# Kernel tuning notes

Measured on AMD Instinct MI355X. Metric: run time of the kernel, lower is better.

The kernel has to match this reference:

```python
import jax, jax.numpy as jnp
import numpy as np

B, C, H, W = 4, 128, 64, 64
NUM_HEADS = 4
HEAD_DIM = C // NUM_HEADS


def setup_inputs() -> dict:
    key = jax.random.key(0)
    ks = jax.random.split(key, 9)
    s = 0.02
    return {
        "x": jax.random.normal(ks[0], (B, C, H, W), dtype=jnp.float32),
        "wq": jax.random.normal(ks[1], (C, C), dtype=jnp.float32) * s,
        "bq": jax.random.normal(ks[2], (C,), dtype=jnp.float32) * s,
        "wk": jax.random.normal(ks[3], (C, C), dtype=jnp.float32) * s,
        "bk": jax.random.normal(ks[4], (C,), dtype=jnp.float32) * s,
        "wv": jax.random.normal(ks[5], (C, C), dtype=jnp.float32) * s,
        "bv": jax.random.normal(ks[6], (C,), dtype=jnp.float32) * s,
        "wo": jax.random.normal(ks[7], (C, C), dtype=jnp.float32) * s,
        "bo": jax.random.normal(ks[8], (C,), dtype=jnp.float32) * s,
    }


def _proj(w, b, xf):
    # 1x1 conv == channel-mixing linear: xf is (B, C, N)
    return jnp.einsum("oc,bcn->bon", w, xf) + b[None, :, None]


def reference(x, wq, bq, wk, bk, wv, bv, wo, bo):
    b, c, h, w = x.shape
    n = h * w
    nh, hd = NUM_HEADS, HEAD_DIM
    xf = x.reshape(b, c, n)
    q = _proj(wq, bq, xf).reshape(b, nh, hd, n)
    k = _proj(wk, bk, xf).reshape(b, nh, hd, n)
    v = _proj(wv, bv, xf).reshape(b, nh, hd, n)
    # scores: (b, heads, n, n)
    scores = jnp.einsum("bhdn,bhdm->bhnm", q, k) / jnp.sqrt(jnp.float32(hd)).astype(x.dtype)
    prob = jax.nn.softmax(scores, axis=-1)
    # attn_out: (b, heads, head_dim, n)
    attn = jnp.einsum("bhnm,bhdm->bhdn", prob, v).reshape(b, c, n)
    out = _proj(wo, bo, attn).reshape(b, c, h, w)
    return x + out
```

## Files before the change

### kernel.cpp

```cpp
#include <hip/hip_runtime.h>
#include <hip/hip_bf16.h>

#define BB 4
#define CC 128
#define NN 4096
#define NHEAD 4
#define HDIM 32
#define KSPLIT 2

typedef short bf16x8_t __attribute__((ext_vector_type(8)));
typedef float f32x4_t __attribute__((ext_vector_type(4)));
typedef int i32x4_t __attribute__((ext_vector_type(4)));

#define MFMA16(a, b, c) __builtin_amdgcn_mfma_f32_16x16x32_bf16(a, b, c, 0, 0, 0)
#define EXP2(x) __builtin_amdgcn_exp2f(x)

#define QSCALE (0.17677669529663687f * 1.4426950408889634f)

static __device__ inline unsigned short f2bf(float f) {
  unsigned u = __builtin_bit_cast(unsigned, f);
  u += 0x7fffu + ((u >> 16) & 1u);
  return (unsigned short)(u >> 16);
}
static __device__ inline unsigned pk2(float lo, float hi) {
  return (unsigned)f2bf(lo) | ((unsigned)f2bf(hi) << 16);
}
static __device__ inline unsigned pack_trunc(float lo, float hi) {
  return __builtin_amdgcn_perm(__builtin_bit_cast(unsigned, hi),
                               __builtin_bit_cast(unsigned, lo), 0x07060302u);
}

static __device__ inline void gload_lds16(const unsigned short* gsrc, void* ldst) {
  __builtin_amdgcn_global_load_lds(
      (const __attribute__((address_space(1))) unsigned int*)gsrc,
      (__attribute__((address_space(3))) unsigned int*)ldst, 16, 0, 0);
}

__global__ __launch_bounds__(256) void wconv_kernel(
    const float* __restrict__ wq, const float* __restrict__ wk,
    const float* __restrict__ wv, const float* __restrict__ wo,
    unsigned short* __restrict__ wb) {
  int f = (blockIdx.x * 256 + threadIdx.x) * 8;
  int m = f >> 14, off = f & 16383;
  const float* src = (m == 0) ? wq : (m == 1) ? wk : (m == 2) ? wv : wo;
  float sc = (m == 0) ? QSCALE : 1.0f;
  float4 a = *(const float4*)(src + off);
  float4 b = *(const float4*)(src + off + 4);
  ushort4 u0, u1;
  u0.x = f2bf(a.x * sc); u0.y = f2bf(a.y * sc); u0.z = f2bf(a.z * sc); u0.w = f2bf(a.w * sc);
  u1.x = f2bf(b.x * sc); u1.y = f2bf(b.y * sc); u1.z = f2bf(b.z * sc); u1.w = f2bf(b.w * sc);
  *(ushort4*)(wb + f) = u0;
  *(ushort4*)(wb + f + 4) = u1;
}

__global__ __launch_bounds__(256) void qkv_mfma_kernel(
    const float* __restrict__ x,
    const unsigned short* __restrict__ wqb, const unsigned short* __restrict__ wkb,
    const unsigned short* __restrict__ wvb,
    const float* __restrict__ bq, const float* __restrict__ bk,
    const float* __restrict__ bv,
    unsigned short* __restrict__ qt, unsigned short* __restrict__ kt,
    unsigned short* __restrict__ vg) {
  __shared__ __attribute__((aligned(16))) unsigned short xsb[64][136];
  __shared__ unsigned short vt[128][66];
  const int b = blockIdx.y, nt = blockIdx.x, proj = blockIdx.z;
  const int tid = threadIdx.x;

#pragma unroll
  for (int i = 0; i < 8; i++) {
    int f = tid + 256 * i;
    int c = f >> 4, n4 = (f & 15) * 4;
    float4 v4 = *(const float4*)(x + ((size_t)b * CC + c) * NN + nt * 64 + n4);
    xsb[n4 + 0][c] = f2bf(v4.x);
    xsb[n4 + 1][c] = f2bf(v4.y);
    xsb[n4 + 2][c] = f2bf(v4.z);
    xsb[n4 + 3][c] = f2bf(v4.w);
  }
  __syncthreads();

  const int lane = tid & 63, w = tid >> 6;
  const int l16 = lane & 15, g = lane >> 4;
  const int nl = w * 16;
  const int ngl = nt * 64 + nl;

  bf16x8_t xf[4];
#pragma unroll
  for (int ks = 0; ks < 4; ks++)
    xf[ks] = *(const bf16x8_t*)&xsb[nl + l16][ks * 32 + g * 8];

  const unsigned short* wm = (proj == 0) ? wqb : (proj == 1) ? wkb : wvb;
  const float* bias = (proj == 0) ? bq : (proj == 1) ? bk : bv;
  const float bsc = (proj == 0) ? QSCALE : 1.0f;
  unsigned short* qkdst = proj ? kt : qt;

#pragma unroll
  for (int ot = 0; ot < 8; ot++) {
    f32x4_t acc;
#pragma unroll
    for (int r = 0; r < 4; r++) acc[r] = bias[ot * 16 + g * 4 + r] * bsc;
#pragma unroll
    for (int ks = 0; ks < 4; ks++) {
      bf16x8_t wf = *(const bf16x8_t*)(wm + (size_t)(ot * 16 + l16) * CC + ks * 32 + g * 8);
      acc = MFMA16(wf, xf[ks], acc);
    }
    if (proj < 2) {
      unsigned p0 = pk2(acc[0], acc[1]);
      unsigned p1 = pk2(acc[2], acc[3]);
      unsigned q0 = (unsigned)__shfl_xor((int)p0, 16);
      unsigned q1 = (unsigned)__shfl_xor((int)p1, 16);
      if ((g & 1) == 0) {
        int hh = ot >> 1, dblk = (ot & 1) * 2 + (g >> 1);
        unsigned short* dst =
            qkdst + (((size_t)(b * NHEAD + hh) * 4 + dblk) * NN + ngl + l16) * 8;
        uint4 val = make_uint4(p0, p1, q0, q1);
        *(uint4*)dst = val;
      }
    } else {
#pragma unroll
      for (int r = 0; r < 4; r++) vt[ot * 16 + g * 4 + r][nl + l16] = f2bf(acc[r]);
    }
  }

  if (proj == 2) {
    __syncthreads();
#pragma unroll
    for (int c = 0; c < 4; c++) {
      int cid = c * 256 + tid;
      int hh = cid >> 8, inner = cid & 255;
      int g2 = inner & 3, l16v = (inner >> 2) & 15, fh = inner >> 6;
      int fv = fh >> 1, half = fh & 1;
      int o = hh * 32 + half * 16 + l16v;
      int n0 = fv * 32 + g2 * 4;
      unsigned d0 = *(const unsigned*)&vt[o][n0];
      unsigned d1 = *(const unsigned*)&vt[o][n0 + 2];
      unsigned d2 = *(const unsigned*)&vt[o][n0 + 16];
      unsigned d3 = *(const unsigned*)&vt[o][n0 + 18];
      uint4 val = make_uint4(d0, d1, d2, d3);
      *(uint4*)(vg + (((size_t)(b * NHEAD + hh) * 64 + nt) * 256 + inner) * 8) = val;
    }
  }
}

__global__ __launch_bounds__(256, 4) void attn_mfma5_kernel(
    const unsigned short* __restrict__ qt, const unsigned short* __restrict__ kt,
    const unsigned short* __restrict__ vg,
    float* __restrict__ opart, float* __restrict__ lpart) {
  __shared__ __attribute__((aligned(16))) unsigned short smem[2][4096];

  const int chunk = blockIdx.x & (KSPLIT - 1), nt = blockIdx.x / KSPLIT;
  const int h = blockIdx.y, b = blockIdx.z;
  const int bh = b * NHEAD + h;
  const int tid = threadIdx.x, lane = tid & 63, wid = tid >> 6;
  const int l16 = lane & 15, g = lane >> 4;
  const int nbase = nt * 128 + wid * 32;

  const unsigned short* qb = qt + (size_t)bh * NN * HDIM;
  const unsigned short* kb = kt + (size_t)bh * NN * HDIM;
  const unsigned short* vgb = vg + (size_t)bh * 64 * 2048;

  const bf16x8_t qf0 = *(const bf16x8_t*)(qb + ((size_t)g * NN + nbase + l16) * 8);
  const bf16x8_t qf1 = *(const bf16x8_t*)(qb + ((size_t)g * NN + nbase + 16 + l16) * 8);

  f32x4_t o00 = {0, 0, 0, 0}, o01 = {0, 0, 0, 0};
  f32x4_t o10 = {0, 0, 0, 0}, o11 = {0, 0, 0, 0};
  f32x4_t la = {0, 0, 0, 0}, lb = {0, 0, 0, 0};
  const f32x4_t zf = {0, 0, 0, 0};
  const i32x4_t onesi = {0x3F803F80, 0x3F803F80, 0x3F803F80, 0x3F803F80};
  const bf16x8_t ones = __builtin_bit_cast(bf16x8_t, onesi);

  const int NITER = 64 / KSPLIT;
  const int mt0 = chunk * NITER;

  const unsigned short* ksrc = kb + ((size_t)g * NN + mt0 * 64 + wid * 16 + l16) * 8;
  const unsigned short* vsrc = vgb + (size_t)mt0 * 2048 + (size_t)((wid * 16 + l16) * 4 + g) * 8;

  auto stage = [&](int p, int i) {
    gload_lds16(ksrc + (size_t)i * 512, &smem[p][wid * 512]);
    gload_lds16(vsrc + (size_t)i * 2048, &smem[p][2048 + wid * 512]);
  };

  auto body = [&](int p) {
    const unsigned short* sk = &smem[p][0];
    bf16x8_t k0 = *(const bf16x8_t*)(sk + 0 * 512 + lane * 8);
    bf16x8_t k1 = *(const bf16x8_t*)(sk + 1 * 512 + lane * 8);
    bf16x8_t k2 = *(const bf16x8_t*)(sk + 2 * 512 + lane * 8);
    bf16x8_t k3 = *(const bf16x8_t*)(sk + 3 * 512 + lane * 8);
    bf16x8_t vf0 = *(const bf16x8_t*)(sk + 2048 + 0 * 512 + lane * 8);
    bf16x8_t vf2 = *(const bf16x8_t*)(sk + 2048 + 1 * 512 + lane * 8);
    bf16x8_t vf1 = *(const bf16x8_t*)(sk + 2048 + 2 * 512 + lane * 8);
    bf16x8_t vf3 = *(const bf16x8_t*)(sk + 2048 + 3 * 512 + lane * 8);

    f32x4_t sA0 = MFMA16(k0, qf0, zf), sA1 = MFMA16(k1, qf0, zf);
    f32x4_t sA2 = MFMA16(k2, qf0, zf), sA3 = MFMA16(k3, qf0, zf);
    f32x4_t sB0 = MFMA16(k0, qf1, zf), sB1 = MFMA16(k1, qf1, zf);
    f32x4_t sB2 = MFMA16(k2, qf1, zf), sB3 = MFMA16(k3, qf1, zf);

#pragma unroll
    for (int r = 0; r < 4; r++) {
      sA0[r] = EXP2(sA0[r]); sA1[r] = EXP2(sA1[r]);
      sA2[r] = EXP2(sA2[r]); sA3[r] = EXP2(sA3[r]);
      sB0[r] = EXP2(sB0[r]); sB1[r] = EXP2(sB1[r]);
      sB2[r] = EXP2(sB2[r]); sB3[r] = EXP2(sB3[r]);
    }

    i32x4_t pA0i = {(int)pack_trunc(sA0[0], sA0[1]), (int)pack_trunc(sA0[2], sA0[3]),
                    (int)pack_trunc(sA1[0], sA1[1]), (int)pack_trunc(sA1[2], sA1[3])};
    i32x4_t pA1i = {(int)pack_trunc(sA2[0], sA2[1]), (int)pack_trunc(sA2[2], sA2[3]),
                    (int)pack_trunc(sA3[0], sA3[1]), (int)pack_trunc(sA3[2], sA3[3])};
    i32x4_t pB0i = {(int)pack_trunc(sB0[0], sB0[1]), (int)pack_trunc(sB0[2], sB0[3]),
                    (int)pack_trunc(sB1[0], sB1[1]), (int)pack_trunc(sB1[2], sB1[3])};
    i32x4_t pB1i = {(int)pack_trunc(sB2[0], sB2[1]), (int)pack_trunc(sB2[2], sB2[3]),
                    (int)pack_trunc(sB3[0], sB3[1]), (int)pack_trunc(sB3[2], sB3[3])};
    bf16x8_t pA0 = __builtin_bit_cast(bf16x8_t, pA0i);
    bf16x8_t pA1 = __builtin_bit_cast(bf16x8_t, pA1i);
    bf16x8_t pB0 = __builtin_bit_cast(bf16x8_t, pB0i);
    bf16x8_t pB1 = __builtin_bit_cast(bf16x8_t, pB1i);

    o00 = MFMA16(vf0, pA0, o00); o00 = MFMA16(vf1, pA1, o00);
    o01 = MFMA16(vf2, pA0, o01); o01 = MFMA16(vf3, pA1, o01);
    o10 = MFMA16(vf0, pB0, o10); o10 = MFMA16(vf1, pB1, o10);
    o11 = MFMA16(vf2, pB0, o11); o11 = MFMA16(vf3, pB1, o11);

    la = MFMA16(ones, pA0, la); la = MFMA16(ones, pA1, la);
    lb = MFMA16(ones, pB0, lb); lb = MFMA16(ones, pB1, lb);
  };

  stage(0, 0);
  __syncthreads();
  for (int mi = 0; mi < NITER; mi += 2) {
    stage(1, mi + 1);
    body(0);
    __syncthreads();
    if (mi + 2 < NITER) stage(0, mi + 2);
    body(1);
    __syncthreads();
  }

  float* obase = opart + ((size_t)(chunk * BB * NHEAD + bh)) * HDIM * NN;
#pragma unroll
  for (int r = 0; r < 4; r++) {
    obase[(size_t)(g * 4 + r) * NN + nbase + l16] = o00[r];
    obase[(size_t)(16 + g * 4 + r) * NN + nbase + l16] = o01[r];
    obase[(size_t)(g * 4 + r) * NN + nbase + 16 + l16] = o10[r];
    obase[(size_t)(16 + g * 4 + r) * NN + nbase + 16 + l16] = o11[r];
  }
  if (g == 0) {
    float* lb_ = lpart + (size_t)(chunk * BB * NHEAD + bh) * NN;
    lb_[nbase + l16] = la[0];
    lb_[nbase + 16 + l16] = lb[0];
  }
}

__global__ __launch_bounds__(256) void combine_kernel(
    const float* __restrict__ opart, const float* __restrict__ lpart,
    unsigned short* __restrict__ attnT) {
  const int n = blockIdx.x * 256 + threadIdx.x;
  const int bh = blockIdx.y, dg = blockIdx.z;
  const int b = bh >> 2, h = bh & 3;

  float l = 0.f;
#pragma unroll
  for (int c = 0; c < KSPLIT; c++) l += lpart[(size_t)(c * BB * NHEAD + bh) * NN + n];
  float inv = 1.f / l;

  unsigned dw[4];
#pragma unroll
  for (int p = 0; p < 4; p++) {
    float s0 = 0.f, s1 = 0.f;
#pragma unroll
    for (int c = 0; c < KSPLIT; c++) {
      const float* ob = opart + ((size_t)(c * BB * NHEAD + bh) * HDIM + dg * 8) * NN;
      s0 += ob[(size_t)(2 * p) * NN + n];
      s1 += ob[(size_t)(2 * p + 1) * NN + n];
    }
    dw[p] = (unsigned)f2bf(s0 * inv) | ((unsigned)f2bf(s1 * inv) << 16);
  }
  unsigned short* dst = attnT + ((size_t)b * NN + n) * CC + h * HDIM + dg * 8;
  *(uint4*)dst = *(uint4*)&dw[0];
}

__global__ __launch_bounds__(256) void out_mfma_kernel(
    const unsigned short* __restrict__ attnT, const unsigned short* __restrict__ wob,
    const float* __restrict__ bo, const float* __restrict__ x,
    float* __restrict__ out) {
  const int b = blockIdx.y, nt = blockIdx.x, quarter = blockIdx.z;
  const int tid = threadIdx.x, lane = tid & 63, w = tid >> 6;
  const int l16 = lane & 15, g = lane >> 4;
  const int n0 = nt * 64 + w * 16;

  bf16x8_t bf[4];
#pragma unroll
  for (int ks = 0; ks < 4; ks++)
    bf[ks] = *(const bf16x8_t*)(attnT + ((size_t)b * NN + n0 + l16) * CC + ks * 32 + g * 8);

#pragma unroll
  for (int mi = 0; mi < 2; mi++) {
    int mt = quarter * 2 + mi;
    f32x4_t acc;
#pragma unroll
    for (int r = 0; r < 4; r++) acc[r] = bo[mt * 16 + g * 4 + r];
#pragma unroll
    for (int ks = 0; ks < 4; ks++) {
      bf16x8_t af = *(const bf16x8_t*)(wob + (size_t)(mt * 16 + l16) * CC + ks * 32 + g * 8);
      acc = MFMA16(af, bf[ks], acc);
    }
#pragma unroll
    for (int r = 0; r < 4; r++) {
      int o = mt * 16 + g * 4 + r;
      size_t addr = ((size_t)b * CC + o) * NN + n0 + l16;
      out[addr] = acc[r] + x[addr];
    }
  }
}

extern "C" void kernel_launch(void* const* d_in, const int* in_sizes, int n_in,
                              void* d_out, int out_size, void* d_ws, size_t ws_size,
                              hipStream_t stream) {
  const float* x  = (const float*)d_in[0];
  const float* wq = (const float*)d_in[1];
  const float* bq = (const float*)d_in[2];
  const float* wk = (const float*)d_in[3];
  const float* bk = (const float*)d_in[4];
  const float* wv = (const float*)d_in[5];
  const float* bv = (const float*)d_in[6];
  const float* wo = (const float*)d_in[7];
  const float* bo = (const float*)d_in[8];
  float* out = (float*)d_out;

  char* w = (char*)d_ws;
  const size_t SZ = (size_t)BB * NHEAD * NN * HDIM * 2;
  unsigned short* qt    = (unsigned short*)w;
  unsigned short* kt    = (unsigned short*)(w + SZ);
  unsigned short* vg    = (unsigned short*)(w + 2 * SZ);
  unsigned short* wb    = (unsigned short*)(w + 3 * SZ);
  float* opart = (float*)(w + 3 * SZ + 131072);
  float* lpart = (float*)(w + 3 * SZ + 131072 +
                          (size_t)KSPLIT * BB * NHEAD * HDIM * NN * 4);
  unsigned short* attnT = qt;
  unsigned short* wqb = wb, *wkb = wb + 16384, *wvb = wb + 32768, *wob = wb + 49152;

  wconv_kernel<<<32, 256, 0, stream>>>(wq, wk, wv, wo, wb);
  qkv_mfma_kernel<<<dim3(NN / 64, BB, 3), 256, 0, stream>>>(
      x, wqb, wkb, wvb, bq, bk, bv, qt, kt, vg);
  attn_mfma5_kernel<<<dim3((NN / 128) * KSPLIT, NHEAD, BB), 256, 0, stream>>>(
      qt, kt, vg, opart, lpart);
  combine_kernel<<<dim3(NN / 256, BB * NHEAD, 4), 256, 0, stream>>>(opart, lpart, attnT);
  out_mfma_kernel<<<dim3(NN / 64, BB, 4), 256, 0, stream>>>(attnT, wob, bo, x, out);
}
```

Measured before the change: 147.0 us.

## Fuse split-K combine into output projection and precompute bf16 transposed x

Merges the combine kernel into the output-projection kernel: each 512-thread block sums the two split-K partials, normalizes by the summed softmax denominators, and stages the bf16 tile in shared memory before the MFMA. This removes a launch and the attnT round trip through global memory. Separately, x is converted to transposed bf16 once in a new xconv kernel, instead of being reconverted by each of the three projection blocks. That adds a launch and a bf16 copy of x, which reuses the opart buffer before the attention kernel overwrites it.

```diff
diff --git a/kernel.cpp b/kernel.cpp
--- a/kernel.cpp
+++ b/kernel.cpp
@@ -53,40 +53,52 @@
   *(ushort4*)(wb + f + 4) = u1;
 }
 
+__global__ __launch_bounds__(256) void xconv_kernel(
+    const float* __restrict__ x, unsigned short* __restrict__ xbT) {
+  __shared__ __attribute__((aligned(16))) unsigned short xs[64][136];
+  const int b = blockIdx.y, nt = blockIdx.x;
+  const int tid = threadIdx.x;
+#pragma unroll
+  for (int i = 0; i < 8; i++) {
+    int f = tid + 256 * i;
+    int c = f >> 4, n4 = (f & 15) * 4;
+    float4 v4 = *(const float4*)(x + ((size_t)b * CC + c) * NN + nt * 64 + n4);
+    xs[n4 + 0][c] = f2bf(v4.x);
+    xs[n4 + 1][c] = f2bf(v4.y);
+    xs[n4 + 2][c] = f2bf(v4.z);
+    xs[n4 + 3][c] = f2bf(v4.w);
+  }
+  __syncthreads();
+  unsigned short* dst = xbT + ((size_t)b * NN + nt * 64) * CC;
+#pragma unroll
+  for (int i = 0; i < 4; i++) {
+    int f = tid + 256 * i;
+    int n = f >> 4, c0 = (f & 15) * 8;
+    *(uint4*)(dst + f * 8) = *(const uint4*)&xs[n][c0];
+  }
+}
+
 __global__ __launch_bounds__(256) void qkv_mfma_kernel(
-    const float* __restrict__ x,
+    const unsigned short* __restrict__ xbT,
     const unsigned short* __restrict__ wqb, const unsigned short* __restrict__ wkb,
     const unsigned short* __restrict__ wvb,
     const float* __restrict__ bq, const float* __restrict__ bk,
     const float* __restrict__ bv,
     unsigned short* __restrict__ qt, unsigned short* __restrict__ kt,
     unsigned short* __restrict__ vg) {
-  __shared__ __attribute__((aligned(16))) unsigned short xsb[64][136];
   __shared__ unsigned short vt[128][66];
   const int b = blockIdx.y, nt = blockIdx.x, proj = blockIdx.z;
   const int tid = threadIdx.x;
-
-#pragma unroll
-  for (int i = 0; i < 8; i++) {
-    int f = tid + 256 * i;
-    int c = f >> 4, n4 = (f & 15) * 4;
-    float4 v4 = *(const float4*)(x + ((size_t)b * CC + c) * NN + nt * 64 + n4);
-    xsb[n4 + 0][c] = f2bf(v4.x);
-    xsb[n4 + 1][c] = f2bf(v4.y);
-    xsb[n4 + 2][c] = f2bf(v4.z);
-    xsb[n4 + 3][c] = f2bf(v4.w);
-  }
-  __syncthreads();
-
   const int lane = tid & 63, w = tid >> 6;
   const int l16 = lane & 15, g = lane >> 4;
   const int nl = w * 16;
   const int ngl = nt * 64 + nl;
 
+  const unsigned short* xrow = xbT + ((size_t)b * NN + ngl + l16) * CC + g * 8;
   bf16x8_t xf[4];
 #pragma unroll
   for (int ks = 0; ks < 4; ks++)
-    xf[ks] = *(const bf16x8_t*)&xsb[nl + l16][ks * 32 + g * 8];
+    xf[ks] = *(const bf16x8_t*)(xrow + ks * 32);
 
   const unsigned short* wm = (proj == 0) ? wqb : (proj == 1) ? wkb : wvb;
   const float* bias = (proj == 0) ? bq : (proj == 1) ? bk : bv;
@@ -251,58 +263,63 @@
   }
 }
 
-__global__ __launch_bounds__(256) void combine_kernel(
+__global__ __launch_bounds__(512) void out_mfma_kernel(
     const float* __restrict__ opart, const float* __restrict__ lpart,
-    unsigned short* __restrict__ attnT) {
-  const int n = blockIdx.x * 256 + threadIdx.x;
-  const int bh = blockIdx.y, dg = blockIdx.z;
-  const int b = bh >> 2, h = bh & 3;
-
-  float l = 0.f;
-#pragma unroll
-  for (int c = 0; c < KSPLIT; c++) l += lpart[(size_t)(c * BB * NHEAD + bh) * NN + n];
-  float inv = 1.f / l;
-
-  unsigned dw[4];
-#pragma unroll
-  for (int p = 0; p < 4; p++) {
-    float s0 = 0.f, s1 = 0.f;
-#pragma unroll
-    for (int c = 0; c < KSPLIT; c++) {
-      const float* ob = opart + ((size_t)(c * BB * NHEAD + bh) * HDIM + dg * 8) * NN;
-      s0 += ob[(size_t)(2 * p) * NN + n];
-      s1 += ob[(size_t)(2 * p + 1) * NN + n];
-    }
-    dw[p] = (unsigned)f2bf(s0 * inv) | ((unsigned)f2bf(s1 * inv) << 16);
-  }
-  unsigned short* dst = attnT + ((size_t)b * NN + n) * CC + h * HDIM + dg * 8;
-  *(uint4*)dst = *(uint4*)&dw[0];
-}
-
-__global__ __launch_bounds__(256) void out_mfma_kernel(
-    const unsigned short* __restrict__ attnT, const unsigned short* __restrict__ wob,
-    const float* __restrict__ bo, const float* __restrict__ x,
-    float* __restrict__ out) {
-  const int b = blockIdx.y, nt = blockIdx.x, quarter = blockIdx.z;
-  const int tid = threadIdx.x, lane = tid & 63, w = tid >> 6;
+    const unsigned short* __restrict__ wob, const float* __restrict__ bo,
+    const float* __restrict__ x, float* __restrict__ out) {
+  __shared__ __attribute__((aligned(16))) unsigned short xsb[64][136];
+  __shared__ float linv[NHEAD][64];
+  const int b = blockIdx.y, nt = blockIdx.x;
+  const int tid = threadIdx.x;
+
+  if (tid < 256) {
+    int h = tid >> 6, nn = tid & 63;
+    int bh = b * NHEAD + h;
+    float l = 0.f;
+#pragma unroll
+    for (int c = 0; c < KSPLIT; c++)
+      l += lpart[(size_t)(c * BB * NHEAD + bh) * NN + nt * 64 + nn];
+    linv[h][nn] = 1.f / l;
+  }
+  __syncthreads();
+
+  const float* ob = opart + (size_t)b * NHEAD * HDIM * NN;
+  const size_t CH = (size_t)BB * NHEAD * HDIM * NN;
+#pragma unroll
+  for (int i = 0; i < 4; i++) {
+    int s = i * 512 + tid;
+    int cd = s >> 4, n4 = (s & 15) * 4;
+    size_t a = (size_t)cd * NN + nt * 64 + n4;
+    float4 v0 = *(const float4*)(ob + a);
+    float4 v1 = *(const float4*)(ob + CH + a);
+    const float* li = &linv[cd >> 5][n4];
+    xsb[n4 + 0][cd] = f2bf((v0.x + v1.x) * li[0]);
+    xsb[n4 + 1][cd] = f2bf((v0.y + v1.y) * li[1]);
+    xsb[n4 + 2][cd] = f2bf((v0.z + v1.z) * li[2]);
+    xsb[n4 + 3][cd] = f2bf((v0.w + v1.w) * li[3]);
+  }
+  __syncthreads();
+
+  const int lane = tid & 63, w = tid >> 6;
   const int l16 = lane & 15, g = lane >> 4;
-  const int n0 = nt * 64 + w * 16;
-
-  bf16x8_t bf[4];
+  const int nsub = (w & 3) * 16, mtbase = (w >> 2) * 4;
+  const int n0 = nt * 64 + nsub;
+
+  bf16x8_t bfr[4];
 #pragma unroll
   for (int ks = 0; ks < 4; ks++)
-    bf[ks] = *(const bf16x8_t*)(attnT + ((size_t)b * NN + n0 + l16) * CC + ks * 32 + g * 8);
-
-#pragma unroll
-  for (int mi = 0; mi < 2; mi++) {
-    int mt = quarter * 2 + mi;
+    bfr[ks] = *(const bf16x8_t*)&xsb[nsub + l16][ks * 32 + g * 8];
+
+#pragma unroll
+  for (int mi = 0; mi < 4; mi++) {
+    int mt = mtbase + mi;
     f32x4_t acc;
 #pragma unroll
     for (int r = 0; r < 4; r++) acc[r] = bo[mt * 16 + g * 4 + r];
 #pragma unroll
     for (int ks = 0; ks < 4; ks++) {
       bf16x8_t af = *(const bf16x8_t*)(wob + (size_t)(mt * 16 + l16) * CC + ks * 32 + g * 8);
-      acc = MFMA16(af, bf[ks], acc);
+      acc = MFMA16(af, bfr[ks], acc);
     }
 #pragma unroll
     for (int r = 0; r < 4; r++) {
@@ -336,14 +353,15 @@
   float* opart = (float*)(w + 3 * SZ + 131072);
   float* lpart = (float*)(w + 3 * SZ + 131072 +
                           (size_t)KSPLIT * BB * NHEAD * HDIM * NN * 4);
-  unsigned short* attnT = qt;
+  unsigned short* xbT = (unsigned short*)opart;
   unsigned short* wqb = wb, *wkb = wb + 16384, *wvb = wb + 32768, *wob = wb + 49152;
 
   wconv_kernel<<<32, 256, 0, stream>>>(wq, wk, wv, wo, wb);
+  xconv_kernel<<<dim3(NN / 64, BB), 256, 0, stream>>>(x, xbT);
   qkv_mfma_kernel<<<dim3(NN / 64, BB, 3), 256, 0, stream>>>(
-      x, wqb, wkb, wvb, bq, bk, bv, qt, kt, vg);
+      xbT, wqb, wkb, wvb, bq, bk, bv, qt, kt, vg);
   attn_mfma5_kernel<<<dim3((NN / 128) * KSPLIT, NHEAD, BB), 256, 0, stream>>>(
       qt, kt, vg, opart, lpart);
-  combine_kernel<<<dim3(NN / 256, BB * NHEAD, 4), 256, 0, stream>>>(opart, lpart, attnT);
-  out_mfma_kernel<<<dim3(NN / 64, BB, 4), 256, 0, stream>>>(attnT, wob, bo, x, out);
-}
+  out_mfma_kernel<<<dim3(NN / 64, BB), 512, 0, stream>>>(
+      opart, lpart, wob, bo, x, out);
+}
```

After: 145.1 us. About the same (-1.3%).
